# Optimization experiments

Measured on AMD Instinct MI355X. Metric: run time of the kernel, lower is better.

## Reference

```python
import jax, jax.numpy as jnp
import numpy as np

E = 384      # hidden_dim
H = 8        # num_attention_heads
D = E // H   # head_dim = 48


def setup_inputs() -> dict:
    key = jax.random.key(0)
    ks = jax.random.split(key, 11)
    B, S = 4, 2048
    patch_embeds = jax.random.normal(ks[0], (B, S, E), dtype=jnp.float32)
    attention_mask = jax.random.randint(ks[1], (B, S), 0, 2).astype(bool)
    s = 1.0 / np.sqrt(E)
    Wq = jax.random.normal(ks[2], (E, E), dtype=jnp.float32) * s
    bq = jnp.zeros((E,), dtype=jnp.float32)
    Wk = jax.random.normal(ks[3], (E, E), dtype=jnp.float32) * s
    bk = jnp.zeros((E,), dtype=jnp.float32)
    Wv = jax.random.normal(ks[4], (E, E), dtype=jnp.float32) * s
    bv = jnp.zeros((E,), dtype=jnp.float32)
    Wo = jax.random.normal(ks[5], (E, E), dtype=jnp.float32) * s
    bo = jnp.zeros((E,), dtype=jnp.float32)
    return {"patch_embeds": patch_embeds, "attention_mask": attention_mask,
            "Wq": Wq, "bq": bq, "Wk": Wk, "bk": bk,
            "Wv": Wv, "bv": bv, "Wo": Wo, "bo": bo}


def reference(patch_embeds, attention_mask, Wq, bq, Wk, bk, Wv, bv, Wo, bo):
    B, S, _ = patch_embeds.shape
    scale = D ** (-0.5)
    # QKV projections (nn.Linear: x @ W.T + b); W stored as [out,in]
    q = patch_embeds @ Wq.T + bq
    k = patch_embeds @ Wk.T + bk
    v = patch_embeds @ Wv.T + bv
    # [B,S,E] -> [B,H,S,D]
    q = q.reshape(B, S, H, D).transpose(0, 2, 1, 3)
    k = k.reshape(B, S, H, D).transpose(0, 2, 1, 3)
    v = v.reshape(B, S, H, D).transpose(0, 2, 1, 3)
    # scaled dot-product attention with key mask (True = masked)
    scores = jnp.einsum('bhqd,bhkd->bhqk', q, k) * scale
    mask = attention_mask[:, None, None, :]  # [B,1,1,S]
    scores = jnp.where(mask, -jnp.inf, scores)
    weights = jax.nn.softmax(scores, axis=-1)
    out = jnp.einsum('bhqk,bhkd->bhqd', weights, v)
    out = out.transpose(0, 2, 1, 3).reshape(B, S, E)
    return out @ Wo.T + bo
```

## Files before the change

kernel.cpp:

```cpp
#include <hip/hip_runtime.h>
#include <math.h>

#define B_ 4
#define S_ 2048
#define E_ 384
#define H_ 8
#define D_ 48
#define M_ (B_*S_)
#define DP_ 64
constexpr float QK_SCALE = 0.14433756729740643f * 1.4426950408889634f;

typedef __attribute__((ext_vector_type(8))) short short8;
typedef __attribute__((ext_vector_type(4))) float f32x4;
typedef unsigned short u16;

__device__ inline u16 f2bf(float f) {
    unsigned u = __float_as_uint(f);
    return (u16)((u + 0x7FFFu + ((u >> 16) & 1u)) >> 16);
}
__device__ inline float bf2f(u16 h) { return __uint_as_float(((unsigned)h) << 16); }
__device__ inline unsigned pk2(float a, float b) {
    return (unsigned)f2bf(a) | ((unsigned)f2bf(b) << 16);
}
__device__ inline unsigned pk2_fast(float a, float b) {
#if __has_builtin(__builtin_amdgcn_perm)
    unsigned ua = __float_as_uint(a) + 0x8000u;
    unsigned ub = __float_as_uint(b) + 0x8000u;
    return __builtin_amdgcn_perm(ub, ua, 0x07060302u);
#else
    return pk2(a, b);
#endif
}
__device__ inline float fexp2(float x) {
#if __has_builtin(__builtin_amdgcn_exp2f)
    return __builtin_amdgcn_exp2f(x);
#else
    return exp2f(x);
#endif
}
__device__ inline void glld16(const void* g, void* l) {
    __builtin_amdgcn_global_load_lds((const __attribute__((address_space(1))) unsigned int*)g,
                                     (__attribute__((address_space(3))) unsigned int*)l, 16, 0, 0);
}

__global__ __launch_bounds__(256) void conv_x(const float4* __restrict__ src,
                                              uint2* __restrict__ hi,
                                              uint2* __restrict__ lo, int n4) {
    int i = blockIdx.x * 256 + threadIdx.x;
    if (i >= n4) return;
    float4 v = src[i];
    u16 h0 = f2bf(v.x), h1 = f2bf(v.y), h2 = f2bf(v.z), h3 = f2bf(v.w);
    uint2 H, L;
    H.x = (unsigned)h0 | ((unsigned)h1 << 16);
    H.y = (unsigned)h2 | ((unsigned)h3 << 16);
    L.x = pk2(v.x - bf2f(h0), v.y - bf2f(h1));
    L.y = pk2(v.z - bf2f(h2), v.w - bf2f(h3));
    hi[i] = H; lo[i] = L;
}

__global__ __launch_bounds__(256) void conv_w4(const float4* __restrict__ wq,
                                               const float4* __restrict__ wk,
                                               const float4* __restrict__ wv,
                                               const float4* __restrict__ wo,
                                               uint2* __restrict__ out, int n4) {
    int i = blockIdx.x * 256 + threadIdx.x;
    if (i >= n4) return;
    const float4* srcs[4] = {wq, wk, wv, wo};
    #pragma unroll
    for (int j = 0; j < 4; ++j) {
        float4 v = srcs[j][i];
        u16 h0 = f2bf(v.x), h1 = f2bf(v.y), h2 = f2bf(v.z), h3 = f2bf(v.w);
        uint2 H, L;
        H.x = (unsigned)h0 | ((unsigned)h1 << 16);
        H.y = (unsigned)h2 | ((unsigned)h3 << 16);
        L.x = pk2(v.x - bf2f(h0), v.y - bf2f(h1));
        L.y = pk2(v.z - bf2f(h2), v.w - bf2f(h3));
        out[(size_t)(j * 2 + 0) * n4 + i] = H;
        out[(size_t)(j * 2 + 1) * n4 + i] = L;
    }
}

__global__ __launch_bounds__(256) void setpad(const int* __restrict__ mask,
                                              u16* __restrict__ Qp,
                                              u16* __restrict__ Kp) {
    int i = blockIdx.x * 256 + threadIdx.x;
    int bh = i >> 11, s = i & 2047;
    int b  = bh >> 3;
    size_t off = ((size_t)bh * S_ + s) * DP_ + 48;
    Kp[off] = mask[b * S_ + s] ? 0xBF80 : 0;
    Qp[off] = 0x4300;
}

template <int MT>
__device__ __forceinline__ void gemm_core(const u16* __restrict__ xh, const u16* __restrict__ xl,
                                          const u16* __restrict__ wh, const u16* __restrict__ wl,
                                          int m0, int n0, f32x4 acc[MT][4]) {
    __shared__ u16 As[2][MT * 64 * 64];
    __shared__ u16 Ws[2][64 * 64];

    const int t = threadIdx.x, w = t >> 6, lane = t & 63;
    const int ln = lane & 15, quad = lane >> 4;
    const int gr = lane >> 3;
    const int gc = (lane & 7) ^ gr;

    #pragma unroll
    for (int mt = 0; mt < MT; ++mt)
        #pragma unroll
        for (int nt = 0; nt < 4; ++nt)
            acc[mt][nt] = (f32x4){0.f, 0.f, 0.f, 0.f};

    for (int kk = 0; kk < 384; kk += 64) {
        __syncthreads();
        #pragma unroll
        for (int i = 0; i < 2 * MT; ++i) {
            int r0 = w * (16 * MT) + i * 8;
            size_t goff = (size_t)(m0 + r0 + gr) * E_ + kk + gc * 8;
            glld16(xh + goff, &As[0][r0 * 64]);
            glld16(xl + goff, &As[1][r0 * 64]);
        }
        #pragma unroll
        for (int i = 0; i < 2; ++i) {
            int r0 = w * 16 + i * 8;
            size_t goff = (size_t)(n0 + r0 + gr) * E_ + kk + gc * 8;
            glld16(wh + goff, &Ws[0][r0 * 64]);
            glld16(wl + goff, &Ws[1][r0 * 64]);
        }
        __syncthreads();

        #pragma unroll
        for (int ks = 0; ks < 2; ++ks) {
            const int slot = (ks * 4 + quad) ^ (ln & 7);
            short8 ah[MT], al[MT], wfh[4], wfl[4];
            #pragma unroll
            for (int mt = 0; mt < MT; ++mt) {
                int row = w * (16 * MT) + mt * 16 + ln;
                ah[mt] = *reinterpret_cast<const short8*>(&As[0][row * 64 + slot * 8]);
                al[mt] = *reinterpret_cast<const short8*>(&As[1][row * 64 + slot * 8]);
            }
            #pragma unroll
            for (int nt = 0; nt < 4; ++nt) {
                int row = nt * 16 + ln;
                wfh[nt] = *reinterpret_cast<const short8*>(&Ws[0][row * 64 + slot * 8]);
                wfl[nt] = *reinterpret_cast<const short8*>(&Ws[1][row * 64 + slot * 8]);
            }
            #pragma unroll
            for (int mt = 0; mt < MT; ++mt)
                #pragma unroll
                for (int nt = 0; nt < 4; ++nt) {
                    acc[mt][nt] = __builtin_amdgcn_mfma_f32_16x16x32_bf16(ah[mt], wfh[nt], acc[mt][nt], 0, 0, 0);
                    acc[mt][nt] = __builtin_amdgcn_mfma_f32_16x16x32_bf16(al[mt], wfh[nt], acc[mt][nt], 0, 0, 0);
                    acc[mt][nt] = __builtin_amdgcn_mfma_f32_16x16x32_bf16(ah[mt], wfl[nt], acc[mt][nt], 0, 0, 0);
                }
        }
    }
}

__global__ __launch_bounds__(256) void gemm_qkv(const u16* __restrict__ xh, const u16* __restrict__ xl,
                                                const u16* __restrict__ wplanes,
                                                const float* __restrict__ bq, const float* __restrict__ bk,
                                                const float* __restrict__ bv,
                                                u16* __restrict__ Qp, u16* __restrict__ Kp,
                                                u16* __restrict__ Vtp) {
    const int y = blockIdx.y;
    const int wsel = y / 6;
    const int n0 = (y - wsel * 6) * 64;
    const int m0 = blockIdx.x * 128;
    const u16* wh = wplanes + (size_t)wsel * 2 * 147456;
    const u16* wl = wh + 147456;

    f32x4 acc[2][4];
    gemm_core<2>(xh, xl, wh, wl, m0, n0, acc);

    const int t = threadIdx.x, w = t >> 6, lane = t & 63;
    const int ln = lane & 15, quad = lane >> 4;
    const int b  = m0 >> 11;
    const int s_base = (m0 & 2047) + w * 32 + quad * 4;
    const float* bias = (wsel == 0) ? bq : (wsel == 1) ? bk : bv;
    const float scale = (wsel == 0) ? QK_SCALE : 1.0f;

    #pragma unroll
    for (int nt = 0; nt < 4; ++nt) {
        const int col = n0 + nt * 16 + ln;
        const int h   = (col * 683) >> 15;
        const int d   = col - h * 48;
        const float bc = bias[col];
        if (wsel == 2) {
            u16* dst = Vtp + ((size_t)(b * 8 + h) * 48 + d) * 2048;
            #pragma unroll
            for (int mt = 0; mt < 2; ++mt) {
                int s0 = s_base + mt * 16;
                uint2 pk;
                pk.x = pk2(acc[mt][nt][0] + bc, acc[mt][nt][1] + bc);
                pk.y = pk2(acc[mt][nt][2] + bc, acc[mt][nt][3] + bc);
                *reinterpret_cast<uint2*>(dst + s0) = pk;
            }
        } else {
            u16* dst = (wsel == 0) ? Qp : Kp;
            dst += ((size_t)(b * 8 + h) * 2048) * DP_ + d;
            #pragma unroll
            for (int mt = 0; mt < 2; ++mt)
                #pragma unroll
                for (int r = 0; r < 4; ++r) {
                    int s = s_base + mt * 16 + r;
                    dst[(size_t)s * DP_] = f2bf((acc[mt][nt][r] + bc) * scale);
                }
        }
    }
}

__global__ __launch_bounds__(256) void gemm_out(const u16* __restrict__ ah, const u16* __restrict__ al,
                                                const u16* __restrict__ wplanes,
                                                const float* __restrict__ bo, float* __restrict__ out) {
    const int m0 = blockIdx.x * 64, n0 = blockIdx.y * 64;
    const u16* wh = wplanes + (size_t)3 * 2 * 147456;
    const u16* wl = wh + 147456;
    f32x4 acc[1][4];
    gemm_core<1>(ah, al, wh, wl, m0, n0, acc);

    const int t = threadIdx.x, w = t >> 6, lane = t & 63;
    const int ln = lane & 15, quad = lane >> 4;
    #pragma unroll
    for (int nt = 0; nt < 4; ++nt) {
        const int col = n0 + nt * 16 + ln;
        const float bc = bo[col];
        #pragma unroll
        for (int r = 0; r < 4; ++r) {
            size_t row = (size_t)(m0 + w * 16 + quad * 4 + r);
            out[row * E_ + col] = acc[0][nt][r] + bc;
        }
    }
}

__global__ __launch_bounds__(256, 4) void attn_mfma(const u16* __restrict__ Qp,
                                                    const u16* __restrict__ Kp,
                                                    const u16* __restrict__ Vtp,
                                                    u16* __restrict__ AOh,
                                                    u16* __restrict__ AOl) {
    __shared__ __align__(16) u16 QPs[64 * 64];
    __shared__ __align__(16) u16 Ksh[2][64 * 64];
    __shared__ __align__(16) u16 Vt[2][48 * 64];
    __shared__ float linv[4][16];

    const int t    = threadIdx.x;
    const int w    = t >> 6;
    const int lane = t & 63;
    const int ln   = lane & 15;
    const int quad = lane >> 4;
    const int gr   = lane >> 3;
    const int gc   = (lane & 7) ^ gr;
    const int q0   = blockIdx.x * 64;
    const int bh   = blockIdx.y;
    const int b    = bh >> 3, h = bh & 7;
    const int cb   = h * 48;
    const size_t rb = (size_t)b * S_;

    const u16* Qsrc = Qp  + ((size_t)bh * S_ + q0) * DP_;
    const u16* Ksrc = Kp  + (size_t)bh * S_ * DP_;
    const u16* Vsrc = Vtp + (size_t)bh * 48 * 2048;

    const int swz0 = ((quad     ) ^ (ln & 7)) << 3;
    const int swz1 = ((4 + quad ) ^ (ln & 7)) << 3;
    const u16* kA[2][2], *vA[2][2];
    #pragma unroll
    for (int bf = 0; bf < 2; ++bf) {
        kA[bf][0] = &Ksh[bf][ln * 64 + swz0];
        kA[bf][1] = &Ksh[bf][ln * 64 + swz1];
        vA[bf][0] = &Vt[bf][ln * 64 + swz0];
        vA[bf][1] = &Vt[bf][ln * 64 + swz1];
    }
    const int qrow = (w * 16 + ln) * 64;
    const u16* pR0 = &QPs[qrow + swz0];
    const u16* pR1 = &QPs[qrow + swz1];
    u16* pW[4];
    #pragma unroll
    for (int Mt = 0; Mt < 4; ++Mt)
        pW[Mt] = &QPs[qrow + ((((Mt * 2 + (quad >> 1)) ^ (ln & 7)) << 3) | ((quad & 1) << 2))];

    auto stage = [&](int bf, int kt) {
        const int k0 = kt * 64;
        glld16(Ksrc + (size_t)(k0 + w * 16 + gr) * DP_ + gc * 8,     &Ksh[bf][(w * 16) * 64]);
        glld16(Ksrc + (size_t)(k0 + w * 16 + 8 + gr) * DP_ + gc * 8, &Ksh[bf][(w * 16 + 8) * 64]);
        if (w < 3) {
            glld16(Vsrc + (size_t)(w * 16 + gr) * 2048 + k0 + gc * 8,     &Vt[bf][(w * 16) * 64]);
            glld16(Vsrc + (size_t)(w * 16 + 8 + gr) * 2048 + k0 + gc * 8, &Vt[bf][(w * 16 + 8) * 64]);
        }
    };

    glld16(Qsrc + (size_t)(w * 16 + gr) * DP_ + gc * 8,     &QPs[(w * 16) * 64]);
    glld16(Qsrc + (size_t)(w * 16 + 8 + gr) * DP_ + gc * 8, &QPs[(w * 16 + 8) * 64]);
    stage(0, 0);
    __syncthreads();

    short8 qf[2];
    qf[0] = *reinterpret_cast<const short8*>(pR0);
    qf[1] = *reinterpret_cast<const short8*>(pR1);

    f32x4 o[3];
    #pragma unroll
    for (int nt = 0; nt < 3; ++nt) o[nt] = (f32x4){0.f, 0.f, 0.f, 0.f};
    float lq = 0.f;

    auto body = [&](int cur, int nxt, int ktn) {
        if (ktn < 32) stage(nxt, ktn);

        f32x4 sc[4];
        #pragma unroll
        for (int Mt = 0; Mt < 4; ++Mt) {
            short8 kf0 = *reinterpret_cast<const short8*>(kA[cur][0] + Mt * 1024);
            short8 kf1 = *reinterpret_cast<const short8*>(kA[cur][1] + Mt * 1024);
            f32x4 a0 = __builtin_amdgcn_mfma_f32_16x16x32_bf16(kf0, qf[0], (f32x4){0.f,0.f,0.f,0.f}, 0, 0, 0);
            sc[Mt] = __builtin_amdgcn_mfma_f32_16x16x32_bf16(kf1, qf[1], a0, 0, 0, 0);
        }

        #pragma unroll
        for (int Mt = 0; Mt < 4; ++Mt) {
            float p0 = fexp2(sc[Mt][0]);
            float p1 = fexp2(sc[Mt][1]);
            float p2 = fexp2(sc[Mt][2]);
            float p3 = fexp2(sc[Mt][3]);
            lq += (p0 + p1) + (p2 + p3);
            uint2 pk;
            pk.x = pk2_fast(p0, p1);
            pk.y = pk2_fast(p2, p3);
            *reinterpret_cast<uint2*>(pW[Mt]) = pk;
        }

        short8 pa0 = *reinterpret_cast<const short8*>(pR0);
        short8 pa1 = *reinterpret_cast<const short8*>(pR1);
        #pragma unroll
        for (int nt = 0; nt < 3; ++nt) {
            short8 vb0 = *reinterpret_cast<const short8*>(vA[cur][0] + nt * 1024);
            short8 vb1 = *reinterpret_cast<const short8*>(vA[cur][1] + nt * 1024);
            o[nt] = __builtin_amdgcn_mfma_f32_16x16x32_bf16(pa0, vb0, o[nt], 0, 0, 0);
            o[nt] = __builtin_amdgcn_mfma_f32_16x16x32_bf16(pa1, vb1, o[nt], 0, 0, 0);
        }
        __syncthreads();
    };

    for (int kt = 0; kt < 32; kt += 2) {
        body(0, 1, kt + 1);
        body(1, 0, kt + 2);
    }

    lq += __shfl_xor(lq, 16);
    lq += __shfl_xor(lq, 32);
    if (quad == 0) linv[w][ln] = 1.0f / lq;
    __syncthreads();
    f32x4 il = *reinterpret_cast<const f32x4*>(&linv[w][quad * 4]);
    #pragma unroll
    for (int nt = 0; nt < 3; ++nt)
        #pragma unroll
        for (int r = 0; r < 4; ++r) {
            size_t row = rb + q0 + w * 16 + quad * 4 + r;
            size_t idx = row * E_ + cb + nt * 16 + ln;
            float val = o[nt][r] * il[r];
            u16 hv = f2bf(val);
            AOh[idx] = hv;
            AOl[idx] = f2bf(val - bf2f(hv));
        }
}

extern "C" void kernel_launch(void* const* d_in, const int* in_sizes, int n_in,
                              void* d_out, int out_size, void* d_ws, size_t ws_size,
                              hipStream_t stream) {
    (void)in_sizes; (void)n_in; (void)out_size; (void)ws_size;
    const float* x    = (const float*)d_in[0];
    const int*   mask = (const int*)  d_in[1];
    const float* Wq   = (const float*)d_in[2];
    const float* bq   = (const float*)d_in[3];
    const float* Wk   = (const float*)d_in[4];
    const float* bk   = (const float*)d_in[5];
    const float* Wv   = (const float*)d_in[6];
    const float* bv   = (const float*)d_in[7];
    const float* Wo   = (const float*)d_in[8];
    const float* bo   = (const float*)d_in[9];

    const size_t NELEM = (size_t)M_ * E_;
    const size_t WELEM = (size_t)E_ * E_;
    const size_t PEL   = (size_t)B_ * H_ * S_ * DP_;
    u16* ws = (u16*)d_ws;
    u16* xh      = ws;
    u16* xl      = xh + NELEM;
    u16* wplanes = xl + NELEM;
    u16* Qp      = wplanes + 8 * WELEM;
    u16* Kp      = Qp + PEL;
    u16* Vtp     = Kp + PEL;
    u16* AOh     = xh;
    u16* AOl     = xl;

    dim3 blk(256);
    hipMemsetAsync(Qp, 0, PEL * sizeof(u16), stream);
    conv_w4<<<dim3((int)(WELEM / 4 / 256)), blk, 0, stream>>>(
        (const float4*)Wq, (const float4*)Wk, (const float4*)Wv, (const float4*)Wo,
        (uint2*)wplanes, (int)(WELEM / 4));
    conv_x<<<dim3((int)(NELEM / 4 / 256)), blk, 0, stream>>>(
        (const float4*)x, (uint2*)xh, (uint2*)xl, (int)(NELEM / 4));
    setpad<<<dim3(B_ * H_ * S_ / 256), blk, 0, stream>>>(mask, Qp, Kp);

    gemm_qkv<<<dim3(M_ / 128, 18), blk, 0, stream>>>(xh, xl, wplanes, bq, bk, bv, Qp, Kp, Vtp);

    attn_mfma<<<dim3(S_ / 64, B_ * H_), blk, 0, stream>>>(Qp, Kp, Vtp, AOh, AOl);

    gemm_out<<<dim3(M_ / 64, 6), blk, 0, stream>>>(AOh, AOl, wplanes, bo, (float*)d_out);
}
```

Measured before the change: 175.6 us.

## Fuse prep kernels, drop memset, stage QK stores via LDS, double attention query tile

Merges the x conversion, weight conversion and pad-setting kernels into one prep kernel, and replaces the full Q-buffer memset with vectorized writes of only the pad columns. The Q/K epilogue of the QKV GEMM now stages results through shared memory so each thread writes 16-byte rows instead of scattered 2-byte stores. The attention kernel processes 128 queries per block (two 16-row tiles per wave), reusing each K/V fragment load across both tiles, with launch bounds relaxed to 2 blocks per SM. Together these aim to cut launch overhead, memset traffic and uncoalesced stores, and to halve K/V LDS traffic per query, at the cost of higher register and LDS use in attention.

```diff
diff --git a/kernel.cpp b/kernel.cpp
--- a/kernel.cpp
+++ b/kernel.cpp
@@ -43,65 +43,66 @@
                                      (__attribute__((address_space(3))) unsigned int*)l, 16, 0, 0);
 }
 
-__global__ __launch_bounds__(256) void conv_x(const float4* __restrict__ src,
-                                              uint2* __restrict__ hi,
-                                              uint2* __restrict__ lo, int n4) {
-    int i = blockIdx.x * 256 + threadIdx.x;
-    if (i >= n4) return;
-    float4 v = src[i];
-    u16 h0 = f2bf(v.x), h1 = f2bf(v.y), h2 = f2bf(v.z), h3 = f2bf(v.w);
-    uint2 H, L;
-    H.x = (unsigned)h0 | ((unsigned)h1 << 16);
-    H.y = (unsigned)h2 | ((unsigned)h3 << 16);
-    L.x = pk2(v.x - bf2f(h0), v.y - bf2f(h1));
-    L.y = pk2(v.z - bf2f(h2), v.w - bf2f(h3));
-    hi[i] = H; lo[i] = L;
-}
-
-__global__ __launch_bounds__(256) void conv_w4(const float4* __restrict__ wq,
-                                               const float4* __restrict__ wk,
-                                               const float4* __restrict__ wv,
-                                               const float4* __restrict__ wo,
-                                               uint2* __restrict__ out, int n4) {
-    int i = blockIdx.x * 256 + threadIdx.x;
-    if (i >= n4) return;
-    const float4* srcs[4] = {wq, wk, wv, wo};
-    #pragma unroll
-    for (int j = 0; j < 4; ++j) {
-        float4 v = srcs[j][i];
+__global__ __launch_bounds__(256) void prep(const float4* __restrict__ x,
+                                            const int* __restrict__ mask,
+                                            const float4* __restrict__ wq,
+                                            const float4* __restrict__ wk,
+                                            const float4* __restrict__ wv,
+                                            const float4* __restrict__ wo,
+                                            uint2* __restrict__ xhi, uint2* __restrict__ xlo,
+                                            uint2* __restrict__ wplanes,
+                                            u16* __restrict__ Qp, u16* __restrict__ Kp) {
+    const int bx = blockIdx.x, t = threadIdx.x;
+    if (bx < 3072) {
+        int i = bx * 256 + t;
+        float4 v = x[i];
         u16 h0 = f2bf(v.x), h1 = f2bf(v.y), h2 = f2bf(v.z), h3 = f2bf(v.w);
         uint2 H, L;
         H.x = (unsigned)h0 | ((unsigned)h1 << 16);
         H.y = (unsigned)h2 | ((unsigned)h3 << 16);
         L.x = pk2(v.x - bf2f(h0), v.y - bf2f(h1));
         L.y = pk2(v.z - bf2f(h2), v.w - bf2f(h3));
-        out[(size_t)(j * 2 + 0) * n4 + i] = H;
-        out[(size_t)(j * 2 + 1) * n4 + i] = L;
-    }
-}
-
-__global__ __launch_bounds__(256) void setpad(const int* __restrict__ mask,
-                                              u16* __restrict__ Qp,
-                                              u16* __restrict__ Kp) {
-    int i = blockIdx.x * 256 + threadIdx.x;
-    int bh = i >> 11, s = i & 2047;
-    int b  = bh >> 3;
-    size_t off = ((size_t)bh * S_ + s) * DP_ + 48;
-    Kp[off] = mask[b * S_ + s] ? 0xBF80 : 0;
-    Qp[off] = 0x4300;
+        xhi[i] = H; xlo[i] = L;
+    } else if (bx < 3072 + 144) {
+        int i = (bx - 3072) * 256 + t;
+        const int n4 = 36864;
+        const float4* srcs[4] = {wq, wk, wv, wo};
+        #pragma unroll
+        for (int j = 0; j < 4; ++j) {
+            float4 v = srcs[j][i];
+            u16 h0 = f2bf(v.x), h1 = f2bf(v.y), h2 = f2bf(v.z), h3 = f2bf(v.w);
+            uint2 H, L;
+            H.x = (unsigned)h0 | ((unsigned)h1 << 16);
+            H.y = (unsigned)h2 | ((unsigned)h3 << 16);
+            L.x = pk2(v.x - bf2f(h0), v.y - bf2f(h1));
+            L.y = pk2(v.z - bf2f(h2), v.w - bf2f(h3));
+            wplanes[(size_t)(j * 2 + 0) * n4 + i] = H;
+            wplanes[(size_t)(j * 2 + 1) * n4 + i] = L;
+        }
+    } else {
+        int i = (bx - 3216) * 256 + t;
+        int bh = i >> 11, s = i & 2047, b = bh >> 3;
+        size_t off = ((size_t)bh * S_ + s) * DP_ + 48;
+        uint4 qz = {0x00004300u, 0, 0, 0};
+        uint4 kz = {mask[b * S_ + s] ? 0x0000BF80u : 0u, 0, 0, 0};
+        uint4 z  = {0, 0, 0, 0};
+        *reinterpret_cast<uint4*>(Qp + off)     = qz;
+        *reinterpret_cast<uint4*>(Qp + off + 8) = z;
+        *reinterpret_cast<uint4*>(Kp + off)     = kz;
+        *reinterpret_cast<uint4*>(Kp + off + 8) = z;
+    }
 }
 
 template <int MT>
 __device__ __forceinline__ void gemm_core(const u16* __restrict__ xh, const u16* __restrict__ xl,
                                           const u16* __restrict__ wh, const u16* __restrict__ wl,
-                                          int m0, int n0, f32x4 acc[MT][4]) {
-    __shared__ u16 As[2][MT * 64 * 64];
-    __shared__ u16 Ws[2][64 * 64];
-
+                                          int m0, int n0, f32x4 acc[MT][4],
+                                          u16* As, u16* Ws) {
     const int t = threadIdx.x, w = t >> 6, lane = t & 63;
     const int ln = lane & 15, quad = lane >> 4;
     const int gr = lane >> 3;
     const int gc = (lane & 7) ^ gr;
+    const int APL = MT * 4096;
 
     #pragma unroll
     for (int mt = 0; mt < MT; ++mt)
@@ -115,15 +116,15 @@
         for (int i = 0; i < 2 * MT; ++i) {
             int r0 = w * (16 * MT) + i * 8;
             size_t goff = (size_t)(m0 + r0 + gr) * E_ + kk + gc * 8;
-            glld16(xh + goff, &As[0][r0 * 64]);
-            glld16(xl + goff, &As[1][r0 * 64]);
+            glld16(xh + goff, As + r0 * 64);
+            glld16(xl + goff, As + APL + r0 * 64);
         }
         #pragma unroll
         for (int i = 0; i < 2; ++i) {
             int r0 = w * 16 + i * 8;
             size_t goff = (size_t)(n0 + r0 + gr) * E_ + kk + gc * 8;
-            glld16(wh + goff, &Ws[0][r0 * 64]);
-            glld16(wl + goff, &Ws[1][r0 * 64]);
+            glld16(wh + goff, Ws + r0 * 64);
+            glld16(wl + goff, Ws + 4096 + r0 * 64);
         }
         __syncthreads();
 
@@ -134,14 +135,14 @@
             #pragma unroll
             for (int mt = 0; mt < MT; ++mt) {
                 int row = w * (16 * MT) + mt * 16 + ln;
-                ah[mt] = *reinterpret_cast<const short8*>(&As[0][row * 64 + slot * 8]);
-                al[mt] = *reinterpret_cast<const short8*>(&As[1][row * 64 + slot * 8]);
+                ah[mt] = *reinterpret_cast<const short8*>(&As[row * 64 + slot * 8]);
+                al[mt] = *reinterpret_cast<const short8*>(&As[APL + row * 64 + slot * 8]);
             }
             #pragma unroll
             for (int nt = 0; nt < 4; ++nt) {
                 int row = nt * 16 + ln;
-                wfh[nt] = *reinterpret_cast<const short8*>(&Ws[0][row * 64 + slot * 8]);
-                wfl[nt] = *reinterpret_cast<const short8*>(&Ws[1][row * 64 + slot * 8]);
+                wfh[nt] = *reinterpret_cast<const short8*>(&Ws[row * 64 + slot * 8]);
+                wfl[nt] = *reinterpret_cast<const short8*>(&Ws[4096 + row * 64 + slot * 8]);
             }
             #pragma unroll
             for (int mt = 0; mt < MT; ++mt)
@@ -161,6 +162,10 @@
                                                 const float* __restrict__ bv,
                                                 u16* __restrict__ Qp, u16* __restrict__ Kp,
                                                 u16* __restrict__ Vtp) {
+    __shared__ u16 smem[2 * 128 * 64 + 2 * 64 * 64];
+    u16* As = smem;
+    u16* Ws = smem + 2 * 128 * 64;
+
     const int y = blockIdx.y;
     const int wsel = y / 6;
     const int n0 = (y - wsel * 6) * 64;
@@ -169,22 +174,21 @@
     const u16* wl = wh + 147456;
 
     f32x4 acc[2][4];
-    gemm_core<2>(xh, xl, wh, wl, m0, n0, acc);
+    gemm_core<2>(xh, xl, wh, wl, m0, n0, acc, As, Ws);
 
     const int t = threadIdx.x, w = t >> 6, lane = t & 63;
     const int ln = lane & 15, quad = lane >> 4;
     const int b  = m0 >> 11;
-    const int s_base = (m0 & 2047) + w * 32 + quad * 4;
     const float* bias = (wsel == 0) ? bq : (wsel == 1) ? bk : bv;
-    const float scale = (wsel == 0) ? QK_SCALE : 1.0f;
-
-    #pragma unroll
-    for (int nt = 0; nt < 4; ++nt) {
-        const int col = n0 + nt * 16 + ln;
-        const int h   = (col * 683) >> 15;
-        const int d   = col - h * 48;
-        const float bc = bias[col];
-        if (wsel == 2) {
+
+    if (wsel == 2) {
+        const int s_base = (m0 & 2047) + w * 32 + quad * 4;
+        #pragma unroll
+        for (int nt = 0; nt < 4; ++nt) {
+            const int col = n0 + nt * 16 + ln;
+            const int h   = (col * 683) >> 15;
+            const int d   = col - h * 48;
+            const float bc = bias[col];
             u16* dst = Vtp + ((size_t)(b * 8 + h) * 48 + d) * 2048;
             #pragma unroll
             for (int mt = 0; mt < 2; ++mt) {
@@ -194,16 +198,34 @@
                 pk.y = pk2(acc[mt][nt][2] + bc, acc[mt][nt][3] + bc);
                 *reinterpret_cast<uint2*>(dst + s0) = pk;
             }
-        } else {
-            u16* dst = (wsel == 0) ? Qp : Kp;
-            dst += ((size_t)(b * 8 + h) * 2048) * DP_ + d;
+        }
+    } else {
+        const float scale = (wsel == 0) ? QK_SCALE : 1.0f;
+        u16* Tr = smem;
+        __syncthreads();
+        #pragma unroll
+        for (int nt = 0; nt < 4; ++nt) {
+            const float bc = bias[n0 + nt * 16 + ln];
             #pragma unroll
             for (int mt = 0; mt < 2; ++mt)
                 #pragma unroll
                 for (int r = 0; r < 4; ++r) {
-                    int s = s_base + mt * 16 + r;
-                    dst[(size_t)s * DP_] = f2bf((acc[mt][nt][r] + bc) * scale);
+                    int row = w * 32 + mt * 16 + quad * 4 + r;
+                    Tr[row * 76 + nt * 16 + ln] = f2bf((acc[mt][nt][r] + bc) * scale);
                 }
+        }
+        __syncthreads();
+        const int row  = t >> 1, half = t & 1;
+        const int s    = (m0 & 2047) + row;
+        const u16* src = &Tr[row * 76 + half * 32];
+        u16* base = (wsel == 0) ? Qp : Kp;
+        #pragma unroll
+        for (int c = 0; c < 4; ++c) {
+            int gcol = n0 + half * 32 + c * 8;
+            int h = (gcol * 683) >> 15;
+            int d = gcol - h * 48;
+            u16* dst = base + ((size_t)(b * 8 + h) * 2048 + s) * DP_ + d;
+            *reinterpret_cast<uint4*>(dst) = *reinterpret_cast<const uint4*>(src + c * 8);
         }
     }
 }
@@ -211,11 +233,14 @@
 __global__ __launch_bounds__(256) void gemm_out(const u16* __restrict__ ah, const u16* __restrict__ al,
                                                 const u16* __restrict__ wplanes,
                                                 const float* __restrict__ bo, float* __restrict__ out) {
+    __shared__ u16 smem[2 * 64 * 64 + 2 * 64 * 64];
+    u16* As = smem;
+    u16* Ws = smem + 2 * 64 * 64;
     const int m0 = blockIdx.x * 64, n0 = blockIdx.y * 64;
     const u16* wh = wplanes + (size_t)3 * 2 * 147456;
     const u16* wl = wh + 147456;
     f32x4 acc[1][4];
-    gemm_core<1>(ah, al, wh, wl, m0, n0, acc);
+    gemm_core<1>(ah, al, wh, wl, m0, n0, acc, As, Ws);
 
     const int t = threadIdx.x, w = t >> 6, lane = t & 63;
     const int ln = lane & 15, quad = lane >> 4;
@@ -231,15 +256,15 @@
     }
 }
 
-__global__ __launch_bounds__(256, 4) void attn_mfma(const u16* __restrict__ Qp,
+__global__ __launch_bounds__(256, 2) void attn_mfma(const u16* __restrict__ Qp,
                                                     const u16* __restrict__ Kp,
                                                     const u16* __restrict__ Vtp,
                                                     u16* __restrict__ AOh,
                                                     u16* __restrict__ AOl) {
-    __shared__ __align__(16) u16 QPs[64 * 64];
+    __shared__ __align__(16) u16 QPs[128 * 64];
     __shared__ __align__(16) u16 Ksh[2][64 * 64];
     __shared__ __align__(16) u16 Vt[2][48 * 64];
-    __shared__ float linv[4][16];
+    __shared__ float linv[4][32];
 
     const int t    = threadIdx.x;
     const int w    = t >> 6;
@@ -248,7 +273,7 @@
     const int quad = lane >> 4;
     const int gr   = lane >> 3;
     const int gc   = (lane & 7) ^ gr;
-    const int q0   = blockIdx.x * 64;
+    const int q0   = blockIdx.x * 128;
     const int bh   = blockIdx.y;
     const int b    = bh >> 3, h = bh & 7;
     const int cb   = h * 48;
@@ -258,8 +283,8 @@
     const u16* Ksrc = Kp  + (size_t)bh * S_ * DP_;
     const u16* Vsrc = Vtp + (size_t)bh * 48 * 2048;
 
-    const int swz0 = ((quad     ) ^ (ln & 7)) << 3;
-    const int swz1 = ((4 + quad ) ^ (ln & 7)) << 3;
+    const int swz0 = ((quad    ) ^ (ln & 7)) << 3;
+    const int swz1 = ((4 + quad) ^ (ln & 7)) << 3;
     const u16* kA[2][2], *vA[2][2];
     #pragma unroll
     for (int bf = 0; bf < 2; ++bf) {
@@ -268,13 +293,19 @@
         vA[bf][0] = &Vt[bf][ln * 64 + swz0];
         vA[bf][1] = &Vt[bf][ln * 64 + swz1];
     }
-    const int qrow = (w * 16 + ln) * 64;
-    const u16* pR0 = &QPs[qrow + swz0];
-    const u16* pR1 = &QPs[qrow + swz1];
-    u16* pW[4];
-    #pragma unroll
-    for (int Mt = 0; Mt < 4; ++Mt)
-        pW[Mt] = &QPs[qrow + ((((Mt * 2 + (quad >> 1)) ^ (ln & 7)) << 3) | ((quad & 1) << 2))];
+    int qrow[2];
+    const u16 *pR[2][2];
+    u16* pW[2][4];
+    #pragma unroll
+    for (int qt = 0; qt < 2; ++qt) {
+        qrow[qt] = (w * 32 + qt * 16 + ln) * 64;
+        pR[qt][0] = &QPs[qrow[qt] + swz0];
+        pR[qt][1] = &QPs[qrow[qt] + swz1];
+        #pragma unroll
+        for (int Mt = 0; Mt < 4; ++Mt)
+            pW[qt][Mt] = &QPs[qrow[qt] +
+                ((((Mt * 2 + (quad >> 1)) ^ (ln & 7)) << 3) | ((quad & 1) << 2))];
+    }
 
     auto stage = [&](int bf, int kt) {
         const int k0 = kt * 64;
@@ -286,53 +317,73 @@
         }
     };
 
-    glld16(Qsrc + (size_t)(w * 16 + gr) * DP_ + gc * 8,     &QPs[(w * 16) * 64]);
-    glld16(Qsrc + (size_t)(w * 16 + 8 + gr) * DP_ + gc * 8, &QPs[(w * 16 + 8) * 64]);
+    #pragma unroll
+    for (int i = 0; i < 4; ++i) {
+        int r0 = w * 32 + i * 8;
+        glld16(Qsrc + (size_t)(r0 + gr) * DP_ + gc * 8, &QPs[r0 * 64]);
+    }
     stage(0, 0);
     __syncthreads();
 
-    short8 qf[2];
-    qf[0] = *reinterpret_cast<const short8*>(pR0);
-    qf[1] = *reinterpret_cast<const short8*>(pR1);
-
-    f32x4 o[3];
-    #pragma unroll
-    for (int nt = 0; nt < 3; ++nt) o[nt] = (f32x4){0.f, 0.f, 0.f, 0.f};
-    float lq = 0.f;
+    short8 qf[2][2];
+    #pragma unroll
+    for (int qt = 0; qt < 2; ++qt) {
+        qf[qt][0] = *reinterpret_cast<const short8*>(pR[qt][0]);
+        qf[qt][1] = *reinterpret_cast<const short8*>(pR[qt][1]);
+    }
+
+    f32x4 o[2][3];
+    #pragma unroll
+    for (int qt = 0; qt < 2; ++qt)
+        #pragma unroll
+        for (int nt = 0; nt < 3; ++nt) o[qt][nt] = (f32x4){0.f, 0.f, 0.f, 0.f};
+    float lq[2] = {0.f, 0.f};
 
     auto body = [&](int cur, int nxt, int ktn) {
         if (ktn < 32) stage(nxt, ktn);
 
-        f32x4 sc[4];
+        f32x4 sc[4][2];
         #pragma unroll
         for (int Mt = 0; Mt < 4; ++Mt) {
             short8 kf0 = *reinterpret_cast<const short8*>(kA[cur][0] + Mt * 1024);
             short8 kf1 = *reinterpret_cast<const short8*>(kA[cur][1] + Mt * 1024);
-            f32x4 a0 = __builtin_amdgcn_mfma_f32_16x16x32_bf16(kf0, qf[0], (f32x4){0.f,0.f,0.f,0.f}, 0, 0, 0);
-            sc[Mt] = __builtin_amdgcn_mfma_f32_16x16x32_bf16(kf1, qf[1], a0, 0, 0, 0);
-        }
-
-        #pragma unroll
-        for (int Mt = 0; Mt < 4; ++Mt) {
-            float p0 = fexp2(sc[Mt][0]);
-            float p1 = fexp2(sc[Mt][1]);
-            float p2 = fexp2(sc[Mt][2]);
-            float p3 = fexp2(sc[Mt][3]);
-            lq += (p0 + p1) + (p2 + p3);
-            uint2 pk;
-            pk.x = pk2_fast(p0, p1);
-            pk.y = pk2_fast(p2, p3);
-            *reinterpret_cast<uint2*>(pW[Mt]) = pk;
-        }
-
-        short8 pa0 = *reinterpret_cast<const short8*>(pR0);
-        short8 pa1 = *reinterpret_cast<const short8*>(pR1);
+            #pragma unroll
+            for (int qt = 0; qt < 2; ++qt) {
+                f32x4 a0 = __builtin_amdgcn_mfma_f32_16x16x32_bf16(kf0, qf[qt][0], (f32x4){0.f,0.f,0.f,0.f}, 0, 0, 0);
+                sc[Mt][qt] = __builtin_amdgcn_mfma_f32_16x16x32_bf16(kf1, qf[qt][1], a0, 0, 0, 0);
+            }
+        }
+
+        #pragma unroll
+        for (int qt = 0; qt < 2; ++qt)
+            #pragma unroll
+            for (int Mt = 0; Mt < 4; ++Mt) {
+                float p0 = fexp2(sc[Mt][qt][0]);
+                float p1 = fexp2(sc[Mt][qt][1]);
+                float p2 = fexp2(sc[Mt][qt][2]);
+                float p3 = fexp2(sc[Mt][qt][3]);
+                lq[qt] += (p0 + p1) + (p2 + p3);
+                uint2 pk;
+                pk.x = pk2_fast(p0, p1);
+                pk.y = pk2_fast(p2, p3);
+                *reinterpret_cast<uint2*>(pW[qt][Mt]) = pk;
+            }
+
+        short8 pa[2][2];
+        #pragma unroll
+        for (int qt = 0; qt < 2; ++qt) {
+            pa[qt][0] = *reinterpret_cast<const short8*>(pR[qt][0]);
+            pa[qt][1] = *reinterpret_cast<const short8*>(pR[qt][1]);
+        }
         #pragma unroll
         for (int nt = 0; nt < 3; ++nt) {
             short8 vb0 = *reinterpret_cast<const short8*>(vA[cur][0] + nt * 1024);
             short8 vb1 = *reinterpret_cast<const short8*>(vA[cur][1] + nt * 1024);
-            o[nt] = __builtin_amdgcn_mfma_f32_16x16x32_bf16(pa0, vb0, o[nt], 0, 0, 0);
-            o[nt] = __builtin_amdgcn_mfma_f32_16x16x32_bf16(pa1, vb1, o[nt], 0, 0, 0);
+            #pragma unroll
+            for (int qt = 0; qt < 2; ++qt) {
+                o[qt][nt] = __builtin_amdgcn_mfma_f32_16x16x32_bf16(pa[qt][0], vb0, o[qt][nt], 0, 0, 0);
+                o[qt][nt] = __builtin_amdgcn_mfma_f32_16x16x32_bf16(pa[qt][1], vb1, o[qt][nt], 0, 0, 0);
+            }
         }
         __syncthreads();
     };
@@ -342,22 +393,29 @@
         body(1, 0, kt + 2);
     }
 
-    lq += __shfl_xor(lq, 16);
-    lq += __shfl_xor(lq, 32);
-    if (quad == 0) linv[w][ln] = 1.0f / lq;
+    #pragma unroll
+    for (int qt = 0; qt < 2; ++qt) {
+        float l = lq[qt];
+        l += __shfl_xor(l, 16);
+        l += __shfl_xor(l, 32);
+        if (quad == 0) linv[w][qt * 16 + ln] = 1.0f / l;
+    }
     __syncthreads();
-    f32x4 il = *reinterpret_cast<const f32x4*>(&linv[w][quad * 4]);
-    #pragma unroll
-    for (int nt = 0; nt < 3; ++nt)
-        #pragma unroll
-        for (int r = 0; r < 4; ++r) {
-            size_t row = rb + q0 + w * 16 + quad * 4 + r;
-            size_t idx = row * E_ + cb + nt * 16 + ln;
-            float val = o[nt][r] * il[r];
-            u16 hv = f2bf(val);
-            AOh[idx] = hv;
-            AOl[idx] = f2bf(val - bf2f(hv));
-        }
+    #pragma unroll
+    for (int qt = 0; qt < 2; ++qt) {
+        f32x4 il = *reinterpret_cast<const f32x4*>(&linv[w][qt * 16 + quad * 4]);
+        #pragma unroll
+        for (int nt = 0; nt < 3; ++nt)
+            #pragma unroll
+            for (int r = 0; r < 4; ++r) {
+                size_t row = rb + q0 + w * 32 + qt * 16 + quad * 4 + r;
+                size_t idx = row * E_ + cb + nt * 16 + ln;
+                float val = o[qt][nt][r] * il[r];
+                u16 hv = f2bf(val);
+                AOh[idx] = hv;
+                AOl[idx] = f2bf(val - bf2f(hv));
+            }
+    }
 }
 
 extern "C" void kernel_launch(void* const* d_in, const int* in_sizes, int n_in,
@@ -389,17 +447,14 @@
     u16* AOl     = xl;
 
     dim3 blk(256);
-    hipMemsetAsync(Qp, 0, PEL * sizeof(u16), stream);
-    conv_w4<<<dim3((int)(WELEM / 4 / 256)), blk, 0, stream>>>(
+    prep<<<dim3(3472), blk, 0, stream>>>(
+        (const float4*)x, mask,
         (const float4*)Wq, (const float4*)Wk, (const float4*)Wv, (const float4*)Wo,
-        (uint2*)wplanes, (int)(WELEM / 4));
-    conv_x<<<dim3((int)(NELEM / 4 / 256)), blk, 0, stream>>>(
-        (const float4*)x, (uint2*)xh, (uint2*)xl, (int)(NELEM / 4));
-    setpad<<<dim3(B_ * H_ * S_ / 256), blk, 0, stream>>>(mask, Qp, Kp);
+        (uint2*)xh, (uint2*)xl, (uint2*)wplanes, Qp, Kp);
 
     gemm_qkv<<<dim3(M_ / 128, 18), blk, 0, stream>>>(xh, xl, wplanes, bq, bk, bv, Qp, Kp, Vtp);
 
-    attn_mfma<<<dim3(S_ / 64, B_ * H_), blk, 0, stream>>>(Qp, Kp, Vtp, AOh, AOl);
+    attn_mfma<<<dim3(S_ / 128, B_ * H_), blk, 0, stream>>>(Qp, Kp, Vtp, AOh, AOl);
 
     gemm_out<<<dim3(M_ / 64, 6), blk, 0, stream>>>(AOh, AOl, wplanes, bo, (float*)d_out);
 }
```

Result: faster. 165.8 us (-5.6%).
